# Kernel tuning notes

Measured on AMD Instinct MI355X. Metric: run time of the kernel, lower is better.

The kernel has to match this reference:

```python
import jax, jax.numpy as jnp
import numpy as np

H = 512          # hidden_size == input_size
K = 32768        # number of child cell inputs (lattice merge fan-in)


def setup_inputs() -> dict:
    key = jax.random.key(0)
    ks = jax.random.split(key, 8)
    s = 1.0 / np.sqrt(H)  # keep matmul outputs O(1)
    return {
        "input_": jax.random.normal(ks[0], (1, H), dtype=jnp.float32),
        "c_input": jax.random.normal(ks[1], (K, H), dtype=jnp.float32),
        "h_0": jax.random.normal(ks[2], (1, H), dtype=jnp.float32),
        "c_0": jax.random.normal(ks[3], (1, H), dtype=jnp.float32),
        "weight_ih": jax.random.normal(ks[4], (H, 3 * H), dtype=jnp.float32) * s,
        "weight_hh": jax.random.normal(ks[5], (H, 3 * H), dtype=jnp.float32) * s,
        "bias": jnp.zeros((3 * H,), dtype=jnp.float32),
        "alpha_weight_ih": jax.random.normal(ks[6], (H, H), dtype=jnp.float32) * s,
        "alpha_weight_hh": jax.random.normal(ks[7], (H, H), dtype=jnp.float32) * s,
    }


def reference(input_, c_input, h_0, c_0, weight_ih, weight_hh, bias,
              alpha_weight_ih, alpha_weight_hh):
    # Gate pre-activations: addmm(bias, h_0, W_hh) + input_ @ W_ih  -> [1, 3H]
    gates = h_0 @ weight_hh + bias + input_ @ weight_ih
    i, o, g = jnp.split(gates, 3, axis=1)        # each [1, H]
    i = jax.nn.sigmoid(i)
    o = jax.nn.sigmoid(o)
    g = jnp.tanh(g)

    # Variable-child softmax-weighted cell merge (non-empty c_input branch)
    alpha_wi = input_ @ alpha_weight_ih          # [1, H], broadcast over K
    alpha_wh = c_input @ alpha_weight_hh         # [K, H]
    alpha = jax.nn.sigmoid(alpha_wi + alpha_wh)  # [K, H]

    logits = jnp.concatenate([i, alpha], axis=0)  # [K+1, H]
    w = jnp.exp(logits)
    w = w / (w.sum(axis=0, keepdims=True) + 1e-12)

    merge = jnp.concatenate([g, c_input], axis=0)  # [K+1, H]
    c_1 = (merge * w).sum(axis=0, keepdims=True)   # [1, H]
    h_1 = o * jnp.tanh(c_1)                        # [1, H]
    return h_1, c_1
```

## Files before the change

### kernel.cpp

```cpp
#include <hip/hip_runtime.h>
#include <hip/hip_bf16.h>
#include <stdint.h>

#define Hdim 512
#define KC   32768

typedef __hip_bfloat16 bf16;
typedef __attribute__((ext_vector_type(8))) short short8;
typedef __attribute__((ext_vector_type(4))) float float4v;

__device__ __forceinline__ unsigned int pack_bf16_trunc(float e0, float e1) {
  union { float f; unsigned int u; } a, b;
  a.f = e0; b.f = e1;
  return __builtin_amdgcn_perm(b.u, a.u, 0x07060302u);
}

__device__ __forceinline__ unsigned long long pack64(float4v v) {
  return (unsigned long long)pack_bf16_trunc(v[0], v[1])
       | ((unsigned long long)pack_bf16_trunc(v[2], v[3]) << 32);
}

__global__ __launch_bounds__(256) void prep_wt_kernel(
    const float* __restrict__ input_, const float* __restrict__ h_0,
    const float* __restrict__ w_ih, const float* __restrict__ w_hh,
    const float* __restrict__ a_w_ih, const float* __restrict__ a_w_hh,
    float* __restrict__ gates, float* __restrict__ awi, bf16* __restrict__ wt) {
  __shared__ float sh[64 * 65];
  const int t = threadIdx.x;
  const int b = blockIdx.x;
  if (b < 32) {
    const int lane = t & 63, wv = t >> 6;
    float* h0s = sh;
    float* ins = sh + 512;
    float* red = sh + 1024;
    for (int i = t; i < 512; i += 256) { h0s[i] = h_0[i]; ins[i] = input_[i]; }
    __syncthreads();
    float acc = 0.f;
    if (b < 24) {
      const int j = b * 64 + lane;
      const float* whh = w_hh + j;
      const float* wih = w_ih + j;
#pragma unroll 16
      for (int i = 0; i < 128; ++i) {
        const int d = wv * 128 + i;
        acc += h0s[d] * whh[(size_t)d * 1536] + ins[d] * wih[(size_t)d * 1536];
      }
    } else {
      const int j = (b - 24) * 64 + lane;
      const float* wai = a_w_ih + j;
#pragma unroll 16
      for (int i = 0; i < 128; ++i) {
        const int d = wv * 128 + i;
        acc += ins[d] * wai[(size_t)d * Hdim];
      }
    }
    red[wv * 64 + lane] = acc;
    __syncthreads();
    if (t < 64) {
      float s = red[t] + red[64 + t] + red[128 + t] + red[192 + t];
      if (b < 24) gates[b * 64 + t] = s;
      else        awi[(b - 24) * 64 + t] = s;
    }
  } else {
    const int bb = b - 32;
    const int d0 = (bb & 7) * 64, h0 = (bb >> 3) * 64;
    const int tx = t & 63, tw = t >> 6;
    float (*tile)[65] = (float (*)[65])sh;
#pragma unroll
    for (int r = 0; r < 16; ++r) {
      const int row = r * 4 + tw;
      tile[row][tx] = a_w_hh[(size_t)(d0 + row) * Hdim + h0 + tx];
    }
    __syncthreads();
#pragma unroll
    for (int r = 0; r < 16; ++r) {
      const int row = r * 4 + tw;
      wt[(size_t)(h0 + row) * Hdim + d0 + tx] = __float2bfloat16(tile[tx][row]);
    }
  }
}

__global__ __launch_bounds__(256) void gemm_reduce_kernel(
    const float* __restrict__ c_input, const bf16* __restrict__ WT,
    const float* __restrict__ awi,
    float* __restrict__ pw, float* __restrict__ pwc) {
  __shared__ __align__(16) bf16 AsBuf[2][128 * 64];
  __shared__ __align__(16) bf16 BsBuf[2][128 * 64];
  __shared__ float red_w[2][128];
  __shared__ float red_wc[2][128];

  const int tid  = threadIdx.x;
  const int lane = tid & 63;
  const int wave = tid >> 6;
  const int wm   = wave & 1;
  const int wn   = wave >> 1;
  const int lm   = lane & 15;
  const int lq   = lane >> 4;

  const int id     = blockIdx.x;
  const int kk_idx = ((id >> 5) << 3) | (id & 7);
  const int h_idx  = (id >> 3) & 3;
  const int kk0 = kk_idx * 128;
  const int h0  = h_idx * 128;

  char* const As0 = (char*)AsBuf[0];
  char* const As1 = (char*)AsBuf[1];
  char* const Bs0 = (char*)BsBuf[0];
  char* const Bs1 = (char*)BsBuf[1];

  const int sub   = tid & 15;
  const int rbase = tid >> 4;
  const float* aglobS = c_input + (size_t)(kk0 + rbase) * Hdim + sub * 4;
  const int a_lds = rbase * 128 + (((sub >> 1) ^ (rbase & 7)) * 16) + (sub & 1) * 8;

  const int brow0 = wave * 8 + (lane >> 3);
  const int bg    = lane & 7;
  const bf16* bglobS = WT + (size_t)(h0 + brow0) * Hdim + bg * 8;
  const int b_lds = brow0 * 128 + ((bg ^ (lane >> 3)) * 16);

  float4v acc[4][4];
#pragma unroll
  for (int i = 0; i < 4; ++i)
#pragma unroll
    for (int j = 0; j < 4; ++j)
      acc[i][j] = (float4v){0.f, 0.f, 0.f, 0.f};

  {
    float4v ap[8]; short8 bp[4];
#pragma unroll
    for (int j = 0; j < 8; ++j)
      ap[j] = *(const float4v*)(aglobS + j * 16 * Hdim);
#pragma unroll
    for (int r = 0; r < 4; ++r)
      bp[r] = *(const short8*)(bglobS + (size_t)r * 32 * Hdim);
#pragma unroll
    for (int j = 0; j < 8; ++j)
      *(unsigned long long*)(As0 + j * 2048 + a_lds) = pack64(ap[j]);
#pragma unroll
    for (int r = 0; r < 4; ++r)
      *(short8*)(Bs0 + r * 4096 + b_lds) = bp[r];
  }
  __syncthreads();

#define GITER(T, RAs, RBs, WAs, WBs, NOT_LAST)                              \
  do {                                                                      \
    float4v ap[8]; short8 bp[4];                                            \
    if (NOT_LAST) {                                                         \
      const int dn = ((T) + 1) * 64;                                        \
      _Pragma("unroll")                                                     \
      for (int j = 0; j < 8; ++j)                                           \
        ap[j] = *(const float4v*)(aglobS + j * 16 * Hdim + dn);             \
      _Pragma("unroll")                                                     \
      for (int r = 0; r < 4; ++r)                                           \
        bp[r] = *(const short8*)(bglobS + (size_t)r * 32 * Hdim + dn);      \
    }                                                                       \
    __builtin_amdgcn_sched_barrier(0);      \
    __builtin_amdgcn_s_setprio(1);                                          \
    _Pragma("unroll")                                                       \
    for (int ks = 0; ks < 2; ++ks) {                                        \
      short8 a[4], bfr[4];                                                  \
      _Pragma("unroll")                                                     \
      for (int mt = 0; mt < 4; ++mt) {                                      \
        const int row = wm * 64 + mt * 16 + lm;                             \
        a[mt] = *(const short8*)(RAs + row * 128 +                          \
                                 (((ks * 4 + lq) ^ (lm & 7)) * 16));        \
      }                                                                     \
      _Pragma("unroll")                                                     \
      for (int nt = 0; nt < 4; ++nt) {                                      \
        const int row = wn * 64 + nt * 16 + lm;                             \
        bfr[nt] = *(const short8*)(RBs + row * 128 +                        \
                                   (((ks * 4 + lq) ^ (lm & 7)) * 16));      \
      }                                                                     \
      _Pragma("unroll")                                                     \
      for (int mt = 0; mt < 4; ++mt)                                        \
        _Pragma("unroll")                                                   \
        for (int nt = 0; nt < 4; ++nt)                                      \
          acc[mt][nt] = __builtin_amdgcn_mfma_f32_16x16x32_bf16(            \
              a[mt], bfr[nt], acc[mt][nt], 0, 0, 0);                        \
    }                                                                       \
    __builtin_amdgcn_s_setprio(0);                                          \
    __builtin_amdgcn_sched_barrier(0);   \
    if (NOT_LAST) {                                                         \
      _Pragma("unroll")                                                     \
      for (int j = 0; j < 8; ++j)                                           \
        *(unsigned long long*)(WAs + j * 2048 + a_lds) = pack64(ap[j]);     \
      _Pragma("unroll")                                                     \
      for (int r = 0; r < 4; ++r)                                           \
        *(short8*)(WBs + r * 4096 + b_lds) = bp[r];                         \
    }                                                                       \
    __syncthreads();                                                        \
  } while (0)

  GITER(0, As0, Bs0, As1, Bs1, 1);
  GITER(1, As1, Bs1, As0, Bs0, 1);
  GITER(2, As0, Bs0, As1, Bs1, 1);
  GITER(3, As1, Bs1, As0, Bs0, 1);
  GITER(4, As0, Bs0, As1, Bs1, 1);
  GITER(5, As1, Bs1, As0, Bs0, 1);
  GITER(6, As0, Bs0, As1, Bs1, 1);
  GITER(7, As1, Bs1, As0, Bs0, 0);
#undef GITER

  float awi_l[4];
#pragma unroll
  for (int nt = 0; nt < 4; ++nt)
    awi_l[nt] = awi[h0 + wn * 64 + nt * 16 + lm];

  float sw[4] = {0.f, 0.f, 0.f, 0.f}, swc[4] = {0.f, 0.f, 0.f, 0.f};
#pragma unroll
  for (int nt = 0; nt < 4; ++nt) {
    const int h = h0 + wn * 64 + nt * 16 + lm;
#pragma unroll
    for (int mt = 0; mt < 4; ++mt) {
      const int kkb = kk0 + wm * 64 + mt * 16 + lq * 4;
#pragma unroll
      for (int r = 0; r < 4; ++r) {
        float v = acc[mt][nt][r] + awi_l[nt];
        float aval = 1.f / (1.f + __expf(-v));
        float e = __expf(aval);
        float c = c_input[(size_t)(kkb + r) * Hdim + h];
        sw[nt]  += e;
        swc[nt] += e * c;
      }
    }
  }
#pragma unroll
  for (int nt = 0; nt < 4; ++nt) {
    sw[nt]  += __shfl_xor(sw[nt], 16, 64);
    sw[nt]  += __shfl_xor(sw[nt], 32, 64);
    swc[nt] += __shfl_xor(swc[nt], 16, 64);
    swc[nt] += __shfl_xor(swc[nt], 32, 64);
  }
  if (lq == 0) {
#pragma unroll
    for (int nt = 0; nt < 4; ++nt) {
      red_w[wm][wn * 64 + nt * 16 + lm]  = sw[nt];
      red_wc[wm][wn * 64 + nt * 16 + lm] = swc[nt];
    }
  }
  __syncthreads();
  if (tid < 128) {
    pw[(size_t)kk_idx * Hdim + h0 + tid]  = red_w[0][tid] + red_w[1][tid];
    pwc[(size_t)kk_idx * Hdim + h0 + tid] = red_wc[0][tid] + red_wc[1][tid];
  }
}

__global__ __launch_bounds__(256) void finalize_kernel(
    const float* __restrict__ pw, const float* __restrict__ pwc,
    const float* __restrict__ gates, const float* __restrict__ bias,
    float* __restrict__ out) {
  __shared__ float rsw[8][32], rswc[8][32];
  const int t = threadIdx.x;
  const int hl = t & 31, q = t >> 5;
  const int hh = blockIdx.x * 32 + hl;
  float sw = 0.f, swc = 0.f;
#pragma unroll 8
  for (int kb = q * 32; kb < q * 32 + 32; ++kb) {
    sw  += pw[(size_t)kb * Hdim + hh];
    swc += pwc[(size_t)kb * Hdim + hh];
  }
  rsw[q][hl] = sw; rswc[q][hl] = swc;
  __syncthreads();
  if (t < 32) {
    const int h = blockIdx.x * 32 + t;
    sw = 0.f; swc = 0.f;
#pragma unroll
    for (int q2 = 0; q2 < 8; ++q2) { sw += rsw[q2][t]; swc += rswc[q2][t]; }
    float ipre = gates[h] + bias[h];
    float opre = gates[Hdim + h] + bias[Hdim + h];
    float gpre = gates[2 * Hdim + h] + bias[2 * Hdim + h];
    float ei = expf(1.f / (1.f + expf(-ipre)));
    float g  = tanhf(gpre);
    float o  = 1.f / (1.f + expf(-opre));
    float denom = ei + sw + 1e-12f;
    float c1 = (ei * g + swc) / denom;
    float h1 = o * tanhf(c1);
    out[h]        = h1;
    out[Hdim + h] = c1;
  }
}

extern "C" void kernel_launch(void* const* d_in, const int* in_sizes, int n_in,
                              void* d_out, int out_size, void* d_ws, size_t ws_size,
                              hipStream_t stream) {
  const float* input_  = (const float*)d_in[0];
  const float* c_input = (const float*)d_in[1];
  const float* h_0     = (const float*)d_in[2];
  const float* w_ih    = (const float*)d_in[4];
  const float* w_hh    = (const float*)d_in[5];
  const float* bias    = (const float*)d_in[6];
  const float* a_w_ih  = (const float*)d_in[7];
  const float* a_w_hh  = (const float*)d_in[8];

  char* ws = (char*)d_ws;
  float* pw    = (float*)ws;
  float* pwc   = (float*)(ws + 512 * 1024);
  float* gates = (float*)(ws + 1024 * 1024);
  float* awi   = (float*)(ws + 1024 * 1024 + 6144);
  bf16*  WT    = (bf16*)(ws + 1024 * 1024 + 8192);

  hipLaunchKernelGGL(prep_wt_kernel, dim3(96), dim3(256), 0, stream,
                     input_, h_0, w_ih, w_hh, a_w_ih, a_w_hh, gates, awi, WT);
  hipLaunchKernelGGL(gemm_reduce_kernel, dim3(1024), dim3(256), 0, stream,
                     c_input, WT, awi, pw, pwc);
  hipLaunchKernelGGL(finalize_kernel, dim3(8 * 2), dim3(256), 0, stream,
                     pw, pwc, gates, bias, (float*)d_out);
}
```

Before: 145.9 us.

## Fuse finalize into GEMM via last-block atomic ticket per hidden slice

Removes the separate finalize kernel launch. Each GEMM block publishes its partials with agent-scope atomic stores and takes a ticket from a per-h-slice counter. The last of the 256 blocks in a slice reduces all partials and computes h_1/c_1. This saves one launch and the gap between kernels, but the tail reduction is serialized in a single block per slice and atomics are added. Counters are reset by the prep kernel.

```diff
diff --git a/kernel.cpp b/kernel.cpp
--- a/kernel.cpp
+++ b/kernel.cpp
@@ -24,10 +24,12 @@
     const float* __restrict__ input_, const float* __restrict__ h_0,
     const float* __restrict__ w_ih, const float* __restrict__ w_hh,
     const float* __restrict__ a_w_ih, const float* __restrict__ a_w_hh,
-    float* __restrict__ gates, float* __restrict__ awi, bf16* __restrict__ wt) {
+    float* __restrict__ gates, float* __restrict__ awi, bf16* __restrict__ wt,
+    int* __restrict__ counters) {
   __shared__ float sh[64 * 65];
   const int t = threadIdx.x;
   const int b = blockIdx.x;
+  if (b == 0 && t < 4) counters[t] = 0;
   if (b < 32) {
     const int lane = t & 63, wv = t >> 6;
     float* h0s = sh;
@@ -83,11 +85,14 @@
 __global__ __launch_bounds__(256) void gemm_reduce_kernel(
     const float* __restrict__ c_input, const bf16* __restrict__ WT,
     const float* __restrict__ awi,
-    float* __restrict__ pw, float* __restrict__ pwc) {
+    float* __restrict__ pw, float* __restrict__ pwc, int* __restrict__ counters,
+    const float* __restrict__ gates, const float* __restrict__ bias,
+    float* __restrict__ out) {
   __shared__ __align__(16) bf16 AsBuf[2][128 * 64];
   __shared__ __align__(16) bf16 BsBuf[2][128 * 64];
   __shared__ float red_w[2][128];
   __shared__ float red_wc[2][128];
+  __shared__ int tkt_s;
 
   const int tid  = threadIdx.x;
   const int lane = tid & 63;
@@ -240,43 +245,48 @@
   }
   __syncthreads();
   if (tid < 128) {
-    pw[(size_t)kk_idx * Hdim + h0 + tid]  = red_w[0][tid] + red_w[1][tid];
-    pwc[(size_t)kk_idx * Hdim + h0 + tid] = red_wc[0][tid] + red_wc[1][tid];
-  }
-}
-
-__global__ __launch_bounds__(256) void finalize_kernel(
-    const float* __restrict__ pw, const float* __restrict__ pwc,
-    const float* __restrict__ gates, const float* __restrict__ bias,
-    float* __restrict__ out) {
-  __shared__ float rsw[8][32], rswc[8][32];
-  const int t = threadIdx.x;
-  const int hl = t & 31, q = t >> 5;
-  const int hh = blockIdx.x * 32 + hl;
-  float sw = 0.f, swc = 0.f;
+    __hip_atomic_store(&pw[(size_t)kk_idx * Hdim + h0 + tid],
+                       red_w[0][tid] + red_w[1][tid],
+                       __ATOMIC_RELAXED, __HIP_MEMORY_SCOPE_AGENT);
+    __hip_atomic_store(&pwc[(size_t)kk_idx * Hdim + h0 + tid],
+                       red_wc[0][tid] + red_wc[1][tid],
+                       __ATOMIC_RELAXED, __HIP_MEMORY_SCOPE_AGENT);
+  }
+  __syncthreads();
+  if (tid == 0)
+    tkt_s = __hip_atomic_fetch_add(&counters[h_idx], 1,
+                                   __ATOMIC_ACQ_REL, __HIP_MEMORY_SCOPE_AGENT);
+  __syncthreads();
+  if (tkt_s == 255) {
+    const int hl = tid & 127, half = tid >> 7;
+    const int h  = h0 + hl;
+    float s1 = 0.f, s2 = 0.f;
 #pragma unroll 8
-  for (int kb = q * 32; kb < q * 32 + 32; ++kb) {
-    sw  += pw[(size_t)kb * Hdim + hh];
-    swc += pwc[(size_t)kb * Hdim + hh];
-  }
-  rsw[q][hl] = sw; rswc[q][hl] = swc;
-  __syncthreads();
-  if (t < 32) {
-    const int h = blockIdx.x * 32 + t;
-    sw = 0.f; swc = 0.f;
-#pragma unroll
-    for (int q2 = 0; q2 < 8; ++q2) { sw += rsw[q2][t]; swc += rswc[q2][t]; }
-    float ipre = gates[h] + bias[h];
-    float opre = gates[Hdim + h] + bias[Hdim + h];
-    float gpre = gates[2 * Hdim + h] + bias[2 * Hdim + h];
-    float ei = expf(1.f / (1.f + expf(-ipre)));
-    float g  = tanhf(gpre);
-    float o  = 1.f / (1.f + expf(-opre));
-    float denom = ei + sw + 1e-12f;
-    float c1 = (ei * g + swc) / denom;
-    float h1 = o * tanhf(c1);
-    out[h]        = h1;
-    out[Hdim + h] = c1;
+    for (int kb = half * 128; kb < half * 128 + 128; ++kb) {
+      s1 += __hip_atomic_load(&pw[(size_t)kb * Hdim + h],
+                              __ATOMIC_RELAXED, __HIP_MEMORY_SCOPE_AGENT);
+      s2 += __hip_atomic_load(&pwc[(size_t)kb * Hdim + h],
+                              __ATOMIC_RELAXED, __HIP_MEMORY_SCOPE_AGENT);
+    }
+    red_w[half][hl]  = s1;
+    red_wc[half][hl] = s2;
+    __syncthreads();
+    if (tid < 128) {
+      const int hh = h0 + tid;
+      float swt  = red_w[0][tid] + red_w[1][tid];
+      float swct = red_wc[0][tid] + red_wc[1][tid];
+      float ipre = gates[hh] + bias[hh];
+      float opre = gates[Hdim + hh] + bias[Hdim + hh];
+      float gpre = gates[2 * Hdim + hh] + bias[2 * Hdim + hh];
+      float ei = expf(1.f / (1.f + expf(-ipre)));
+      float g  = tanhf(gpre);
+      float o  = 1.f / (1.f + expf(-opre));
+      float denom = ei + swt + 1e-12f;
+      float c1 = (ei * g + swct) / denom;
+      float h1 = o * tanhf(c1);
+      out[hh]        = h1;
+      out[Hdim + hh] = c1;
+    }
   }
 }
 
@@ -298,11 +308,12 @@
   float* gates = (float*)(ws + 1024 * 1024);
   float* awi   = (float*)(ws + 1024 * 1024 + 6144);
   bf16*  WT    = (bf16*)(ws + 1024 * 1024 + 8192);
+  int*   ctrs  = (int*)(ws + 1024 * 1024 + 8192 + 512 * 1024);
 
   hipLaunchKernelGGL(prep_wt_kernel, dim3(96), dim3(256), 0, stream,
-                     input_, h_0, w_ih, w_hh, a_w_ih, a_w_hh, gates, awi, WT);
+                     input_, h_0, w_ih, w_hh, a_w_ih, a_w_hh, gates, awi, WT,
+                     ctrs);
   hipLaunchKernelGGL(gemm_reduce_kernel, dim3(1024), dim3(256), 0, stream,
-                     c_input, WT, awi, pw, pwc);
-  hipLaunchKernelGGL(finalize_kernel, dim3(8 * 2), dim3(256), 0, stream,
-                     pw, pwc, gates, bias, (float*)d_out);
-}
+                     c_input, WT, awi, pw, pwc, ctrs, gates, bias,
+                     (float*)d_out);
+}
```

Result: slower. 183.0 us (+25.4%).
